# Optimization experiments

Hardware: AMD Instinct MI355X
Metric: run time of the kernel (lower is better)

## Reference

```python
import jax, jax.numpy as jnp
import numpy as np

NUM_CLASSES = 100
CLUSTERS_PER_CLASS = 64
LATENT_DIM = 128
BATCH = 32768


def setup_inputs() -> dict:
    key = jax.random.key(0)
    kx, kc, kl = jax.random.split(key, 3)
    x = jax.random.normal(kx, (BATCH, LATENT_DIM), dtype=jnp.float32)
    # nn.Parameter(torch.randn(C, Kc, D) * 0.1)
    centers = jax.random.normal(kc, (NUM_CLASSES, CLUSTERS_PER_CLASS, LATENT_DIM), dtype=jnp.float32) * 0.1
    labels = jax.random.randint(kl, (BATCH,), 0, NUM_CLASSES, dtype=jnp.int64)
    return {"x": x, "centers": centers, "labels": labels}


def reference(x, centers, labels):
    # [C, Kc, D] -> [K, D]
    all_centers = centers.reshape(-1, LATENT_DIM).astype(x.dtype)
    x2 = jnp.sum(x * x, axis=-1, keepdims=True)            # [B,1]
    c2 = jnp.sum(all_centers * all_centers, axis=-1)       # [K]
    sq = x2 + c2[None, :] - 2.0 * jnp.einsum('bd,kd->bk', x, all_centers)
    distances = jnp.sqrt(jnp.maximum(sq, 0.0))             # [B,K]
    closest_indices = jnp.argmin(distances, axis=1)        # [B]
    class_predictions = closest_indices // CLUSTERS_PER_CLASS
    cluster_assignments = closest_indices % CLUSTERS_PER_CLASS
    quantized_hard = all_centers[closest_indices]          # [B,D]
    min_distances = jnp.take_along_axis(distances, closest_indices[:, None], axis=1)[:, 0]
    # straight-through estimator (training path in the torch module)
    quantized = x + jax.lax.stop_gradient(quantized_hard - x)
    return quantized, cluster_assignments, min_distances, class_predictions
```

## Files before the change

kernel.cpp:

```cpp
#include <hip/hip_runtime.h>
#include <math.h>

#define BATCH  32768
#define D      128
#define K      6400
#define KC     64
#define ROWS_PER_BLOCK 64
#define CHUNK_C 64
#define NCHUNKS 100
#define CHUNK_BYTES 16384

typedef _Float16 half8 __attribute__((ext_vector_type(8)));
typedef float    floatx4 __attribute__((ext_vector_type(4)));

typedef __attribute__((address_space(3))) unsigned       lds_uint;
typedef __attribute__((address_space(1))) const unsigned glb_uint;

__device__ __forceinline__ void async_lds16(const void* g, void* l) {
    __builtin_amdgcn_global_load_lds((glb_uint*)g, (lds_uint*)l, 16, 0, 0);
}

__global__ __launch_bounds__(256) void pack_kernel(const float* __restrict__ centers,
                                                   _Float16* __restrict__ wh,
                                                   float* __restrict__ c2n) {
    int tid = blockIdx.x * 256 + threadIdx.x;
    int ch = tid >> 10;
    int u  = (tid >> 6) & 15;
    int cw = tid & 63;
    int center = ch * CHUNK_C + cw;
    const float* src = centers + (size_t)center * D + u * 8;
    float4 a = *(const float4*)src;
    float4 b = *(const float4*)(src + 4);
    float f[8] = {a.x, a.y, a.z, a.w, b.x, b.y, b.z, b.w};
    half8 h;
#pragma unroll
    for (int j = 0; j < 8; ++j) h[j] = (_Float16)f[j];
    *(half8*)(wh + (size_t)tid * 8) = h;

    if (blockIdx.x < K / KC) {
        int c_local = threadIdx.x >> 2, part = threadIdx.x & 3;
        int c = blockIdx.x * 64 + c_local;
        const float4* p = (const float4*)(centers + (size_t)c * D + part * 32);
        float s = 0.f;
#pragma unroll
        for (int i = 0; i < 8; ++i) {
            float4 v = p[i];
            s = fmaf(v.x, v.x, s); s = fmaf(v.y, v.y, s);
            s = fmaf(v.z, v.z, s); s = fmaf(v.w, v.w, s);
        }
        s += __shfl_xor(s, 1, 64);
        s += __shfl_xor(s, 2, 64);
        if (part == 0) c2n[c] = -0.5f * s;
    }
}

__global__ __launch_bounds__(512, 6) void dist_kernel(
    const float* __restrict__ x, const float* __restrict__ centers,
    const _Float16* __restrict__ wh, const float* __restrict__ c2n,
    float* __restrict__ out) {
    __shared__ char bufs[3][CHUNK_BYTES];
    __shared__ int  candL[ROWS_PER_BLOCK * 8];

    const int t    = threadIdx.x;
    const int w    = t >> 6;
    const int L    = t & 63;
    const int quad = L >> 4;
    const int n16  = L & 15;
    const int cq   = w & 3;
    const int rq   = w >> 2;
    const int gr0  = blockIdx.x * ROWS_PER_BLOCK;

    half8 Ah[2][4];
#pragma unroll
    for (int rt = 0; rt < 2; ++rt) {
        int r = gr0 + rq * 32 + rt * 16 + n16;
        const float* xr = x + (size_t)r * D + quad * 8;
#pragma unroll
        for (int ks = 0; ks < 4; ++ks) {
            float4 a = *(const float4*)(xr + ks * 32);
            float4 b = *(const float4*)(xr + ks * 32 + 4);
            float f[8] = {a.x, a.y, a.z, a.w, b.x, b.y, b.z, b.w};
            half8 h;
#pragma unroll
            for (int j = 0; j < 8; ++j) h[j] = (_Float16)f[j];
            Ah[rt][ks] = h;
        }
    }

    float b1[8], b2[8];
#pragma unroll
    for (int k = 0; k < 8; ++k) { b1[k] = -1e30f; b2[k] = -1e30f; }

    const char* gh = (const char*)wh;
    const int laneoff = cq * 16 + n16;

    char* pA = bufs[0];  char* pB = bufs[1];  char* pC = bufs[2];
#pragma unroll
    for (int i = 0; i < 2; ++i) {
        int seg = w + i * 8;
        async_lds16(gh + seg * 1024 + L * 16, pA + seg * 1024);
    }
    float c2cur = c2n[laneoff];
#pragma unroll
    for (int i = 0; i < 2; ++i) {
        int seg = w + i * 8;
        async_lds16(gh + CHUNK_BYTES + seg * 1024 + L * 16, pB + seg * 1024);
    }
    float c2nxt = c2n[CHUNK_C + laneoff];

    for (int ci = 0; ci < NCHUNKS; ++ci) {
        if (ci + 1 < NCHUNKS) { asm volatile("s_waitcnt vmcnt(3)" ::: "memory"); }
        else                  { asm volatile("s_waitcnt vmcnt(0)" ::: "memory"); }
        __builtin_amdgcn_sched_barrier(0);
        __builtin_amdgcn_s_barrier();
        __builtin_amdgcn_sched_barrier(0);

        floatx4 cinit = (floatx4){c2cur, c2cur, c2cur, c2cur};
        const half8* pb = (const half8*)pA + quad * 64 + laneoff;
        floatx4 acc0, acc1;
        __builtin_amdgcn_s_setprio(1);
        {
            half8 Bf = pb[0];
            acc0 = __builtin_amdgcn_mfma_f32_16x16x32_f16(Ah[0][0], Bf, cinit, 0, 0, 0);
            acc1 = __builtin_amdgcn_mfma_f32_16x16x32_f16(Ah[1][0], Bf, cinit, 0, 0, 0);
        }
#pragma unroll
        for (int ks = 1; ks < 4; ++ks) {
            half8 Bf = pb[ks * 256];
            acc0 = __builtin_amdgcn_mfma_f32_16x16x32_f16(Ah[0][ks], Bf, acc0, 0, 0, 0);
            acc1 = __builtin_amdgcn_mfma_f32_16x16x32_f16(Ah[1][ks], Bf, acc1, 0, 0, 0);
        }
        __builtin_amdgcn_s_setprio(0);

        float c2new = 0.f;
        if (ci + 2 < NCHUNKS) {
            const char* gn = gh + (size_t)(ci + 2) * CHUNK_BYTES;
#pragma unroll
            for (int i = 0; i < 2; ++i) {
                int seg = w + i * 8;
                async_lds16(gn + seg * 1024 + L * 16, pC + seg * 1024);
            }
            c2new = c2n[(ci + 2) * CHUNK_C + laneoff];
        }
        c2cur = c2nxt; c2nxt = c2new;

        const unsigned pk = (unsigned)ci;
#pragma unroll
        for (int reg = 0; reg < 4; ++reg) {
            float v0 = __uint_as_float((__float_as_uint(acc0[reg]) & ~127u) | pk);
            b2[reg] = __builtin_amdgcn_fmed3f(b1[reg], b2[reg], v0);
            b1[reg] = fmaxf(b1[reg], v0);
            float v1 = __uint_as_float((__float_as_uint(acc1[reg]) & ~127u) | pk);
            b2[4 + reg] = __builtin_amdgcn_fmed3f(b1[4 + reg], b2[4 + reg], v1);
            b1[4 + reg] = fmaxf(b1[4 + reg], v1);
        }

        char* tmp = pA; pA = pB; pB = pC; pC = tmp;
    }

#pragma unroll
    for (int k = 0; k < 8; ++k) {
        unsigned u1 = __float_as_uint(b1[k]), u2 = __float_as_uint(b2[k]);
        int e1 = (int)(u1 & 127u), e2 = (int)(u2 & 127u);
        int p1 = e1 * CHUNK_C + laneoff;
        int p2 = e2 * CHUNK_C + laneoff;
        float v1 = b1[k], v2 = b2[k];
#pragma unroll
        for (int m = 1; m < 16; m <<= 1) {
            float o1 = __shfl_xor(v1, m, 64), o2 = __shfl_xor(v2, m, 64);
            int   q1 = __shfl_xor(p1, m, 64), q2 = __shfl_xor(p2, m, 64);
            bool firstMine = (v1 > o1) || (v1 == o1 && p1 < q1);
            float nv1 = firstMine ? v1 : o1;  int np1 = firstMine ? p1 : q1;
            float cb  = firstMine ? o1 : v1;  int cpi = firstMine ? q1 : p1;
            float ob  = firstMine ? v2 : o2;  int obi = firstMine ? p2 : q2;
            bool secOwn = (ob > cb) || (ob == cb && obi < cpi);
            v1 = nv1; p1 = np1;
            v2 = secOwn ? ob : cb;  p2 = secOwn ? obi : cpi;
        }
        if (n16 == 0) {
            int rloc = rq * 32 + (k >> 2) * 16 + quad * 4 + (k & 3);
            candL[rloc * 8 + cq * 2 + 0] = p1;
            candL[rloc * 8 + cq * 2 + 1] = p2;
        }
    }
    __syncthreads();

    {
        int r = t >> 3, p = t & 7;
        int row = gr0 + r;
        int ix = candL[r * 8 + p];
        const float4* xr4 = (const float4*)(x + (size_t)row * D);
        const float4* c4  = (const float4*)(centers + (size_t)ix * D);
        float dot = 0.f, x2s = 0.f, c2 = 0.f;
#pragma unroll
        for (int d4 = 0; d4 < 32; ++d4) {
            float4 xv = xr4[d4], cv = c4[d4];
            dot = fmaf(xv.x, cv.x, dot); dot = fmaf(xv.y, cv.y, dot);
            dot = fmaf(xv.z, cv.z, dot); dot = fmaf(xv.w, cv.w, dot);
            x2s = fmaf(xv.x, xv.x, x2s); x2s = fmaf(xv.y, xv.y, x2s);
            x2s = fmaf(xv.z, xv.z, x2s); x2s = fmaf(xv.w, xv.w, x2s);
            c2  = fmaf(cv.x, cv.x, c2);  c2  = fmaf(cv.y, cv.y, c2);
            c2  = fmaf(cv.z, cv.z, c2);  c2  = fmaf(cv.w, cv.w, c2);
        }
        float sq = x2s + c2 - 2.f * dot;
#pragma unroll
        for (int m = 1; m < 8; m <<= 1) {
            float osq = __shfl_xor(sq, m, 64);
            int   oix = __shfl_xor(ix, m, 64);
            if (osq < sq || (osq == sq && oix < ix)) { sq = osq; ix = oix; }
        }

        float* out_clu = out + (size_t)BATCH * D;
        float* out_md  = out_clu + BATCH;
        float* out_cls = out_md + BATCH;
        if (p == 0) {
            out_md[row]  = sqrtf(fmaxf(sq, 0.f));
            out_clu[row] = (float)(ix & (KC - 1));
            out_cls[row] = (float)(ix >> 6);
        }

        const float4* cv4 = (const float4*)(centers + (size_t)ix * D) + p * 4;
        const float4* xv4 = (const float4*)(x + (size_t)row * D) + p * 4;
        float4* o4 = (float4*)(out + (size_t)row * D) + p * 4;
#pragma unroll
        for (int i = 0; i < 4; ++i) {
            float4 cv = cv4[i], xv = xv4[i];
            float4 o;
            o.x = xv.x + (cv.x - xv.x);
            o.y = xv.y + (cv.y - xv.y);
            o.z = xv.z + (cv.z - xv.z);
            o.w = xv.w + (cv.w - xv.w);
            o4[i] = o;
        }
    }
}

extern "C" void kernel_launch(void* const* d_in, const int* in_sizes, int n_in,
                              void* d_out, int out_size, void* d_ws, size_t ws_size,
                              hipStream_t stream) {
    const float* x       = (const float*)d_in[0];
    const float* centers = (const float*)d_in[1];
    float* out = (float*)d_out;

    _Float16* wh  = (_Float16*)d_ws;
    float*    c2n = (float*)(wh + (size_t)K * D);

    pack_kernel<<<(K * 16) / 256, 256, 0, stream>>>(centers, wh, c2n);
    dist_kernel<<<BATCH / ROWS_PER_BLOCK, 512, 0, stream>>>(x, centers, wh, c2n, out);
}
```

Measured before the change: 189.7 us.

## Give each wave a private double-buffered center tile to drop block barriers

Each wave now streams its own 16-center fp16 tile into a private double buffer in LDS, so the per-chunk block-wide s_barrier is gone and only a per-wave vmcnt wait remains. The pack kernel is relaid so each 16-center tile is contiguous. The aim is to let waves run out of lockstep and stop stalling on block synchronisation. In exchange, waves that share a center column but handle different rows now load the same tile twice, LDS per block grows to 64KB, and launch bounds drop from 6 to 4 waves per SIMD, which lowers occupancy.

```diff
diff --git a/kernel.cpp b/kernel.cpp
--- a/kernel.cpp
+++ b/kernel.cpp
@@ -6,9 +6,9 @@
 #define K      6400
 #define KC     64
 #define ROWS_PER_BLOCK 64
-#define CHUNK_C 64
-#define NCHUNKS 100
-#define CHUNK_BYTES 16384
+#define UNIT_C 64
+#define NU     100
+#define TILE_BYTES 4096
 
 typedef _Float16 half8 __attribute__((ext_vector_type(8)));
 typedef float    floatx4 __attribute__((ext_vector_type(4)));
@@ -24,10 +24,10 @@
                                                    _Float16* __restrict__ wh,
                                                    float* __restrict__ c2n) {
     int tid = blockIdx.x * 256 + threadIdx.x;
-    int ch = tid >> 10;
-    int u  = (tid >> 6) & 15;
-    int cw = tid & 63;
-    int center = ch * CHUNK_C + cw;
+    int T   = tid >> 8;
+    int u   = (tid >> 4) & 15;
+    int c16 = tid & 15;
+    int center = T * 16 + c16;
     const float* src = centers + (size_t)center * D + u * 8;
     float4 a = *(const float4*)src;
     float4 b = *(const float4*)(src + 4);
@@ -54,12 +54,11 @@
     }
 }
 
-__global__ __launch_bounds__(512, 6) void dist_kernel(
+__global__ __launch_bounds__(512, 4) void dist_kernel(
     const float* __restrict__ x, const float* __restrict__ centers,
     const _Float16* __restrict__ wh, const float* __restrict__ c2n,
     float* __restrict__ out) {
-    __shared__ char bufs[3][CHUNK_BYTES];
-    __shared__ int  candL[ROWS_PER_BLOCK * 8];
+    __shared__ char lds[65536];
 
     const int t    = threadIdx.x;
     const int w    = t >> 6;
@@ -69,6 +68,9 @@
     const int cq   = w & 3;
     const int rq   = w >> 2;
     const int gr0  = blockIdx.x * ROWS_PER_BLOCK;
+    const int laneC = cq * 16 + n16;
+
+    char* wbuf = lds + w * 8192;
 
     half8 Ah[2][4];
 #pragma unroll
@@ -91,60 +93,42 @@
 #pragma unroll
     for (int k = 0; k < 8; ++k) { b1[k] = -1e30f; b2[k] = -1e30f; }
 
-    const char* gh = (const char*)wh;
-    const int laneoff = cq * 16 + n16;
-
-    char* pA = bufs[0];  char* pB = bufs[1];  char* pC = bufs[2];
-#pragma unroll
-    for (int i = 0; i < 2; ++i) {
-        int seg = w + i * 8;
-        async_lds16(gh + seg * 1024 + L * 16, pA + seg * 1024);
-    }
-    float c2cur = c2n[laneoff];
-#pragma unroll
-    for (int i = 0; i < 2; ++i) {
-        int seg = w + i * 8;
-        async_lds16(gh + CHUNK_BYTES + seg * 1024 + L * 16, pB + seg * 1024);
-    }
-    float c2nxt = c2n[CHUNK_C + laneoff];
-
-    for (int ci = 0; ci < NCHUNKS; ++ci) {
-        if (ci + 1 < NCHUNKS) { asm volatile("s_waitcnt vmcnt(3)" ::: "memory"); }
-        else                  { asm volatile("s_waitcnt vmcnt(0)" ::: "memory"); }
+    const char* gh = (const char*)wh + (size_t)cq * TILE_BYTES;
+
+#pragma unroll
+    for (int i = 0; i < 4; ++i)
+        async_lds16(gh + i * 1024 + L * 16, wbuf + i * 1024);
+    float c2cur = c2n[laneC];
+
+    for (int u = 0; u < NU; ++u) {
+        char* curb = wbuf + (u & 1) * TILE_BYTES;
+        float c2nxt = 0.f;
+        if (u + 1 < NU) {
+            const char* gn = gh + (size_t)(u + 1) * (4 * TILE_BYTES);
+            char* nxtb = wbuf + ((u + 1) & 1) * TILE_BYTES;
+#pragma unroll
+            for (int i = 0; i < 4; ++i)
+                async_lds16(gn + i * 1024 + L * 16, nxtb + i * 1024);
+            c2nxt = c2n[(u + 1) * UNIT_C + laneC];
+            asm volatile("s_waitcnt vmcnt(5)" ::: "memory");
+        } else {
+            asm volatile("s_waitcnt vmcnt(0)" ::: "memory");
+        }
         __builtin_amdgcn_sched_barrier(0);
-        __builtin_amdgcn_s_barrier();
-        __builtin_amdgcn_sched_barrier(0);
-
-        floatx4 cinit = (floatx4){c2cur, c2cur, c2cur, c2cur};
-        const half8* pb = (const half8*)pA + quad * 64 + laneoff;
-        floatx4 acc0, acc1;
+
+        floatx4 acc0 = (floatx4){c2cur, c2cur, c2cur, c2cur};
+        floatx4 acc1 = acc0;
+
         __builtin_amdgcn_s_setprio(1);
-        {
-            half8 Bf = pb[0];
-            acc0 = __builtin_amdgcn_mfma_f32_16x16x32_f16(Ah[0][0], Bf, cinit, 0, 0, 0);
-            acc1 = __builtin_amdgcn_mfma_f32_16x16x32_f16(Ah[1][0], Bf, cinit, 0, 0, 0);
-        }
-#pragma unroll
-        for (int ks = 1; ks < 4; ++ks) {
-            half8 Bf = pb[ks * 256];
+#pragma unroll
+        for (int ks = 0; ks < 4; ++ks) {
+            half8 Bf = *(const half8*)(curb + (((ks * 4 + quad) * 16 + n16) << 4));
             acc0 = __builtin_amdgcn_mfma_f32_16x16x32_f16(Ah[0][ks], Bf, acc0, 0, 0, 0);
             acc1 = __builtin_amdgcn_mfma_f32_16x16x32_f16(Ah[1][ks], Bf, acc1, 0, 0, 0);
         }
         __builtin_amdgcn_s_setprio(0);
 
-        float c2new = 0.f;
-        if (ci + 2 < NCHUNKS) {
-            const char* gn = gh + (size_t)(ci + 2) * CHUNK_BYTES;
-#pragma unroll
-            for (int i = 0; i < 2; ++i) {
-                int seg = w + i * 8;
-                async_lds16(gn + seg * 1024 + L * 16, pC + seg * 1024);
-            }
-            c2new = c2n[(ci + 2) * CHUNK_C + laneoff];
-        }
-        c2cur = c2nxt; c2nxt = c2new;
-
-        const unsigned pk = (unsigned)ci;
+        const unsigned pk = (unsigned)u;
 #pragma unroll
         for (int reg = 0; reg < 4; ++reg) {
             float v0 = __uint_as_float((__float_as_uint(acc0[reg]) & ~127u) | pk);
@@ -155,15 +139,18 @@
             b1[4 + reg] = fmaxf(b1[4 + reg], v1);
         }
 
-        char* tmp = pA; pA = pB; pB = pC; pC = tmp;
-    }
+        c2cur = c2nxt;
+    }
+
+    __syncthreads();
+    int* candL = (int*)lds;
 
 #pragma unroll
     for (int k = 0; k < 8; ++k) {
         unsigned u1 = __float_as_uint(b1[k]), u2 = __float_as_uint(b2[k]);
         int e1 = (int)(u1 & 127u), e2 = (int)(u2 & 127u);
-        int p1 = e1 * CHUNK_C + laneoff;
-        int p2 = e2 * CHUNK_C + laneoff;
+        int p1 = e1 * UNIT_C + laneC;
+        int p2 = e2 * UNIT_C + laneC;
         float v1 = b1[k], v2 = b2[k];
 #pragma unroll
         for (int m = 1; m < 16; m <<= 1) {
```

Measured after the change: 195.3 us. 3.0% more time.
